# Kernel optimization log

Measured on AMD Instinct MI355X. Metric: run time of the kernel, lower is better.

## Reference

```python
import jax, jax.numpy as jnp
import numpy as np

D_MODEL = 1024
N_HEADS = 16
HEAD_DIM = D_MODEL // N_HEADS
D_FF = 4 * D_MODEL
LN_EPS = 1e-5  # torch nn.LayerNorm default


def setup_inputs() -> dict:
    key = jax.random.key(0)
    ks = jax.random.split(key, 6)
    B, T = 2, 2048
    s = lambda fan_in: 1.0 / np.sqrt(fan_in)
    return {
        "x": jax.random.normal(ks[0], (B, T, D_MODEL), dtype=jnp.float32),
        # weights stored as [in, out]
        "w_qkv": jax.random.normal(ks[1], (D_MODEL, 3 * D_MODEL), dtype=jnp.float32) * s(D_MODEL),
        "w_proj": jax.random.normal(ks[2], (D_MODEL, D_MODEL), dtype=jnp.float32) * s(D_MODEL),
        "ln1_g": jnp.ones((D_MODEL,), jnp.float32),
        "ln1_b": jnp.zeros((D_MODEL,), jnp.float32),
        "ln2_g": jnp.ones((D_MODEL,), jnp.float32),
        "ln2_b": jnp.zeros((D_MODEL,), jnp.float32),
        "w_ff1": jax.random.normal(ks[3], (D_MODEL, D_FF), dtype=jnp.float32) * s(D_MODEL),
        "b_ff1": jnp.zeros((D_FF,), jnp.float32),
        "w_ff2": jax.random.normal(ks[4], (D_FF, D_MODEL), dtype=jnp.float32) * s(D_FF),
        "b_ff2": jnp.zeros((D_MODEL,), jnp.float32),
    }


def _layernorm(x, g, b):
    mu = jnp.mean(x, axis=-1, keepdims=True)
    var = jnp.mean(jnp.square(x - mu), axis=-1, keepdims=True)
    return (x - mu) * jax.lax.rsqrt(var + LN_EPS) * g + b


def _attention(x, w_qkv, w_proj):
    B, T, C = x.shape
    qkv = x @ w_qkv  # [B,T,3C]
    q, k, v = jnp.split(qkv, 3, axis=-1)
    # [B, H, T, Dh]
    q = q.reshape(B, T, N_HEADS, HEAD_DIM).transpose(0, 2, 1, 3)
    k = k.reshape(B, T, N_HEADS, HEAD_DIM).transpose(0, 2, 1, 3)
    v = v.reshape(B, T, N_HEADS, HEAD_DIM).transpose(0, 2, 1, 3)
    att = jnp.einsum("bhqd,bhkd->bhqk", q, k) / np.sqrt(HEAD_DIM).astype(np.float32)
    causal = jnp.tril(jnp.ones((T, T), dtype=bool))
    att = jnp.where(causal, att, -jnp.inf)
    att = jax.nn.softmax(att, axis=-1)
    y = jnp.einsum("bhqk,bhkd->bhqd", att, v)
    y = y.transpose(0, 2, 1, 3).reshape(B, T, C)
    return y @ w_proj


def _ffn(x, w1, b1, w2, b2):
    h = jax.nn.gelu(x @ w1 + b1, approximate=False)  # torch nn.GELU default is exact
    return h @ w2 + b2


def reference(x, w_qkv, w_proj, ln1_g, ln1_b, ln2_g, ln2_b, w_ff1, b_ff1, w_ff2, b_ff2):
    x = x + _attention(_layernorm(x, ln1_g, ln1_b), w_qkv, w_proj)
    x = x + _ffn(_layernorm(x, ln2_g, ln2_b), w_ff1, b_ff1, w_ff2, b_ff2)
    return x
```

## Files before the change

### kernel.cpp

```cpp
#include <hip/hip_runtime.h>
#include <hip/hip_bf16.h>

typedef unsigned short u16;
typedef unsigned int u32;
typedef unsigned long long u64;
typedef __bf16 bf16x8 __attribute__((ext_vector_type(8)));
typedef float f32x4 __attribute__((ext_vector_type(4)));
typedef u16 u16x8 __attribute__((ext_vector_type(8)));

#define LN_EPS 1e-5f
#define SCALE_L2E 0.18033688011112042f

__device__ inline float bf2f(u16 u) { return __uint_as_float(((u32)u) << 16); }
__device__ inline u16 f2b(float f) {
    u32 u = __float_as_uint(f);
    u32 r = (u + 0x7fffu + ((u >> 16) & 1u)) >> 16;
    return (u16)r;
}
__device__ inline u32 cvtpk(float a, float b) {
    u32 r;
    asm("v_cvt_pk_bf16_f32 %0, %1, %2" : "=v"(r) : "v"(a), "v"(b));
    return r;
}

typedef __attribute__((address_space(3))) u32 as3_u32;
typedef const __attribute__((address_space(1))) u32 as1_u32;
__device__ inline void gl_lds16(const u16* g, u16* l) {
    __builtin_amdgcn_global_load_lds((as1_u32*)g, (as3_u32*)l, 16, 0, 0);
}

__global__ __launch_bounds__(256) void cast_transpose_k(const float* __restrict__ W,
                                                        u16* __restrict__ WT, int K, int N) {
    __shared__ float tile[64][65];
    int n0 = blockIdx.x * 64, k0 = blockIdx.y * 64;
    int t = threadIdx.x;
#pragma unroll
    for (int i = 0; i < 4; i++) {
        int idx = t + i * 256;
        int r = idx >> 4;
        int cq = idx & 15;
        float4 v = *reinterpret_cast<const float4*>(&W[(size_t)(k0 + r) * N + n0 + cq * 4]);
        tile[r][cq * 4 + 0] = v.x; tile[r][cq * 4 + 1] = v.y;
        tile[r][cq * 4 + 2] = v.z; tile[r][cq * 4 + 3] = v.w;
    }
    __syncthreads();
#pragma unroll
    for (int i = 0; i < 2; i++) {
        int c = t + i * 256;
        int n = c >> 3;
        int k8 = (c & 7) * 8;
        u16x8 o;
#pragma unroll
        for (int j = 0; j < 8; j++) o[j] = f2b(tile[k8 + j][n]);
        *reinterpret_cast<u16x8*>(&WT[(size_t)(n0 + n) * K + k0 + k8]) = o;
    }
}

__global__ __launch_bounds__(256) void layernorm_k(const float* __restrict__ X,
                                                   const float* __restrict__ g,
                                                   const float* __restrict__ b,
                                                   u16* __restrict__ out) {
    int row = blockIdx.x;
    int t = threadIdx.x;
    float4 v = *reinterpret_cast<const float4*>(&X[(size_t)row * 1024 + t * 4]);
    float s = v.x + v.y + v.z + v.w;
    float s2 = v.x * v.x + v.y * v.y + v.z * v.z + v.w * v.w;
#pragma unroll
    for (int o = 1; o < 64; o <<= 1) {
        s += __shfl_xor(s, o, 64);
        s2 += __shfl_xor(s2, o, 64);
    }
    __shared__ float ws[4], ws2[4];
    int wid = t >> 6, lane = t & 63;
    if (lane == 0) { ws[wid] = s; ws2[wid] = s2; }
    __syncthreads();
    float ts = ws[0] + ws[1] + ws[2] + ws[3];
    float ts2 = ws2[0] + ws2[1] + ws2[2] + ws2[3];
    float mu = ts * (1.0f / 1024.0f);
    float var = ts2 * (1.0f / 1024.0f) - mu * mu;
    float rs = rsqrtf(var + LN_EPS);
    float4 gg = *reinterpret_cast<const float4*>(&g[t * 4]);
    float4 bb = *reinterpret_cast<const float4*>(&b[t * 4]);
    u16 o4[4];
    o4[0] = f2b((v.x - mu) * rs * gg.x + bb.x);
    o4[1] = f2b((v.y - mu) * rs * gg.y + bb.y);
    o4[2] = f2b((v.z - mu) * rs * gg.z + bb.z);
    o4[3] = f2b((v.w - mu) * rs * gg.w + bb.w);
    *reinterpret_cast<ulonglong1*>(&out[(size_t)row * 1024 + t * 4]) =
        *reinterpret_cast<ulonglong1*>(o4);
}

template<int BN>
__global__ __launch_bounds__(256) void gemm_k(const u16* __restrict__ A,
                                              const u16* __restrict__ Bt,
                                              int M, int N, int K,
                                              const float* __restrict__ bias,
                                              const float* __restrict__ resid,
                                              int do_gelu,
                                              float* __restrict__ outF,
                                              u16* __restrict__ outB) {
    constexpr int NI = BN / 32;
    __shared__ u16 As[2][128 * 32];
    __shared__ u16 Bs[2][BN * 32];
    int gx = gridDim.x;
    int nwg = gx * gridDim.y;
    int id = blockIdx.y * gx + blockIdx.x;
    int id2 = (nwg & 7) ? id : ((id & 7) * (nwg >> 3) + (id >> 3));
    int bx = id2 % gx, by = id2 / gx;
    int m0 = by * 128, n0 = bx * BN;
    int t = threadIdx.x;
    int w = t >> 6, lane = t & 63;
    int lr = lane & 15, lg = lane >> 4;
    int wm = (w >> 1) * 64, wn = (w & 1) * (BN / 2);
    f32x4 acc[4][NI] = {};

    auto stage = [&](int buf, int k0) {
#pragma unroll
        for (int i = 0; i < 2; i++) {
            int c = t + i * 256;
            int row = c >> 2, pch = c & 3;
            gl_lds16(&A[(size_t)(m0 + row) * K + k0 + ((pch ^ ((row >> 1) & 3)) * 8)],
                     &As[buf][c * 8]);
        }
#pragma unroll
        for (int i = 0; i < BN / 64; i++) {
            int c = t + i * 256;
            int row = c >> 2, pch = c & 3;
            gl_lds16(&Bt[(size_t)(n0 + row) * K + k0 + ((pch ^ ((row >> 1) & 3)) * 8)],
                     &Bs[buf][c * 8]);
        }
    };

    stage(0, 0);
    __syncthreads();
    int cur = 0;
    for (int k0 = 0; k0 < K; k0 += 32) {
        if (k0 + 32 < K) stage(cur ^ 1, k0 + 32);
        bf16x8 af[4], bfr[NI];
#pragma unroll
        for (int mi = 0; mi < 4; mi++) {
            int row = wm + mi * 16 + lr;
            af[mi] = *reinterpret_cast<const bf16x8*>(&As[cur][row * 32 + ((lg ^ ((row >> 1) & 3)) * 8)]);
        }
#pragma unroll
        for (int ni = 0; ni < NI; ni++) {
            int row = wn + ni * 16 + lr;
            bfr[ni] = *reinterpret_cast<const bf16x8*>(&Bs[cur][row * 32 + ((lg ^ ((row >> 1) & 3)) * 8)]);
        }
        __builtin_amdgcn_s_setprio(1);
#pragma unroll
        for (int mi = 0; mi < 4; mi++)
#pragma unroll
            for (int ni = 0; ni < NI; ni++)
                acc[mi][ni] = __builtin_amdgcn_mfma_f32_16x16x32_bf16(af[mi], bfr[ni], acc[mi][ni], 0, 0, 0);
        __builtin_amdgcn_s_setprio(0);
        __syncthreads();
        cur ^= 1;
    }
#pragma unroll
    for (int mi = 0; mi < 4; mi++) {
#pragma unroll
        for (int ni = 0; ni < NI; ni++) {
            int col = n0 + wn + ni * 16 + lr;
#pragma unroll
            for (int i = 0; i < 4; i++) {
                int row = m0 + wm + mi * 16 + lg * 4 + i;
                float v = acc[mi][ni][i];
                if (bias) v += bias[col];
                if (do_gelu) v = 0.5f * v * (1.0f + erff(v * 0.70710678118f));
                if (resid) v += resid[(size_t)row * N + col];
                if (outF) outF[(size_t)row * N + col] = v;
                else outB[(size_t)row * N + col] = f2b(v);
            }
        }
    }
}

__global__ __launch_bounds__(256) void attn_k(const u16* __restrict__ QKV, u16* __restrict__ Y) {
    __shared__ u16 Ks[64 * 64];
    __shared__ u16 Vt[64 * 64];
    __shared__ u16 Pt[4][16 * 64];
    int u = (blockIdx.x + blockIdx.y) & 31;
    int vv = (u & 8) ? (u ^ 7) : u;
    int qt = 31 - vv;
    int bh = blockIdx.y;
    int b = bh >> 4, h = bh & 15;
    int t = threadIdx.x;
    int w = t >> 6, lane = t & 63;
    int lr = lane & 15, lg = lane >> 4;
    int q_g = qt * 64 + w * 16 + lr;
    size_t bhbase = (size_t)b * 2048 * 3072 + h * 64;

    bf16x8 qf[2];
#pragma unroll
    for (int ks = 0; ks < 2; ks++)
        qf[ks] = *reinterpret_cast<const bf16x8*>(&QKV[bhbase + (size_t)q_g * 3072 + ks * 32 + lg * 8]);

    float m = -1e30f, l = 0.0f;
    f32x4 oacc[4] = {};

    int vkey = t & 63;
    int vd0 = (t >> 6) * 8;
    int nkv = qt + 1;

    for (int kt = 0; kt < nkv; kt++) {
        size_t tb = bhbase + (size_t)(kt * 64) * 3072;
#pragma unroll
        for (int i = 0; i < 2; i++) {
            int c = t + i * 256;
            int key = c >> 3, pch = c & 7;
            gl_lds16(&QKV[tb + (size_t)key * 3072 + 1024 + ((pch ^ (key & 7)) * 8)], &Ks[c * 8]);
        }
        u16x8 vreg[2];
#pragma unroll
        for (int i = 0; i < 2; i++)
            vreg[i] = *reinterpret_cast<const u16x8*>(&QKV[tb + (size_t)vkey * 3072 + 2048 + vd0 + i * 32]);
#pragma unroll
        for (int i = 0; i < 2; i++)
#pragma unroll
            for (int j = 0; j < 8; j++) {
                int d = vd0 + i * 32 + j;
                Vt[(d * 64 + vkey) ^ ((d & 7) << 3)] = vreg[i][j];
            }
        __syncthreads();

        int kbmax = (kt == qt) ? (w + 1) : 4;
        f32x4 s[4];
        __builtin_amdgcn_s_setprio(1);
#pragma unroll
        for (int kb = 0; kb < 4; kb++) {
            if (kb < kbmax) {
                int key = kb * 16 + lr;
                bf16x8 k0 = *reinterpret_cast<const bf16x8*>(&Ks[key * 64 + ((lg ^ (key & 7)) * 8)]);
                bf16x8 k1 = *reinterpret_cast<const bf16x8*>(&Ks[key * 64 + (((4 + lg) ^ (key & 7)) * 8)]);
                f32x4 z = {0, 0, 0, 0};
                z = __builtin_amdgcn_mfma_f32_16x16x32_bf16(k0, qf[0], z, 0, 0, 0);
                s[kb] = __builtin_amdgcn_mfma_f32_16x16x32_bf16(k1, qf[1], z, 0, 0, 0);
            }
        }
        __builtin_amdgcn_s_setprio(0);

        float p[16];
        float mt = -1e30f;
        bool diag = (kt == qt);
#pragma unroll
        for (int kb = 0; kb < 4; kb++) {
            if (kb < kbmax) {
#pragma unroll
                for (int i2 = 0; i2 < 4; i2++) {
                    float v = s[kb][i2] * SCALE_L2E;
                    if (diag && kb == w)
                        v = (kb * 16 + lg * 4 + i2 <= w * 16 + lr) ? v : -1e30f;
                    p[kb * 4 + i2] = v;
                    mt = fmaxf(mt, v);
                }
            }
        }
        mt = fmaxf(mt, __shfl_xor(mt, 16, 64));
        mt = fmaxf(mt, __shfl_xor(mt, 32, 64));
        float mn = fmaxf(m, mt);
        float scf = exp2f(m - mn);
        float ps = 0.0f;
#pragma unroll
        for (int kb = 0; kb < 4; kb++) {
            if (kb < kbmax) {
#pragma unroll
                for (int i2 = 0; i2 < 4; i2++) {
                    float e = exp2f(p[kb * 4 + i2] - mn);
                    p[kb * 4 + i2] = e;
                    ps += e;
                }
            }
        }
        ps += __shfl_xor(ps, 16, 64);
        ps += __shfl_xor(ps, 32, 64);
        l = l * scf + ps;
        m = mn;
#pragma unroll
        for (int db = 0; db < 4; db++) {
            oacc[db][0] *= scf; oacc[db][1] *= scf;
            oacc[db][2] *= scf; oacc[db][3] *= scf;
        }
#pragma unroll
        for (int kb = 0; kb < 4; kb++) {
            u32 d0 = 0, d1 = 0;
            if (kb < kbmax) {
                d0 = cvtpk(p[kb * 4 + 0], p[kb * 4 + 1]);
                d1 = cvtpk(p[kb * 4 + 2], p[kb * 4 + 3]);
            }
            int eidx = (lr * 64 + kb * 16 + lg * 4) ^ ((lr & 7) << 3);
            *reinterpret_cast<u64*>(&Pt[w][eidx]) = (u64)d0 | ((u64)d1 << 32);
        }
        __builtin_amdgcn_s_setprio(1);
#pragma unroll
        for (int ks = 0; ks < 2; ks++) {
            bf16x8 pb = *reinterpret_cast<const bf16x8*>(&Pt[w][(lr * 64 + ks * 32 + lg * 8) ^ ((lr & 7) << 3)]);
#pragma unroll
            for (int db = 0; db < 4; db++) {
                int d = db * 16 + lr;
                bf16x8 va = *reinterpret_cast<const bf16x8*>(&Vt[(d * 64 + ks * 32 + lg * 8) ^ ((d & 7) << 3)]);
                oacc[db] = __builtin_amdgcn_mfma_f32_16x16x32_bf16(va, pb, oacc[db], 0, 0, 0);
            }
        }
        __builtin_amdgcn_s_setprio(0);
        __syncthreads();
    }

    float inv = 1.0f / l;
#pragma unroll
    for (int db = 0; db < 4; db++) {
        u32 lo = cvtpk(oacc[db][0] * inv, oacc[db][1] * inv);
        u32 hi = cvtpk(oacc[db][2] * inv, oacc[db][3] * inv);
        size_t ya = (size_t)(b * 2048 + q_g) * 1024 + h * 64 + db * 16 + lg * 4;
        *reinterpret_cast<u32*>(&Y[ya]) = lo;
        *reinterpret_cast<u32*>(&Y[ya + 2]) = hi;
    }
}

extern "C" void kernel_launch(void* const* d_in, const int* in_sizes, int n_in,
                              void* d_out, int out_size, void* d_ws, size_t ws_size,
                              hipStream_t stream) {
    const float* x      = (const float*)d_in[0];
    const float* w_qkv  = (const float*)d_in[1];
    const float* w_proj = (const float*)d_in[2];
    const float* ln1_g  = (const float*)d_in[3];
    const float* ln1_b  = (const float*)d_in[4];
    const float* ln2_g  = (const float*)d_in[5];
    const float* ln2_b  = (const float*)d_in[6];
    const float* w_ff1  = (const float*)d_in[7];
    const float* b_ff1  = (const float*)d_in[8];
    const float* w_ff2  = (const float*)d_in[9];
    const float* b_ff2  = (const float*)d_in[10];
    float* out = (float*)d_out;

    char* ws = (char*)d_ws;
    u16* qkv    = (u16*)(ws);
    u16* act16  = (u16*)(ws + 25165824);
    float* x2   = (float*)(ws + 33554432);
    u16* hbuf   = (u16*)(ws + 50331648);
    u16* wqkvT  = (u16*)(ws + 83886080);
    u16* wprojT = (u16*)(ws + 90177536);
    u16* wff1T  = (u16*)(ws + 92274688);
    u16* wff2T  = (u16*)(ws + 100663296);

    cast_transpose_k<<<dim3(48, 16), 256, 0, stream>>>(w_qkv, wqkvT, 1024, 3072);
    cast_transpose_k<<<dim3(16, 16), 256, 0, stream>>>(w_proj, wprojT, 1024, 1024);
    cast_transpose_k<<<dim3(64, 16), 256, 0, stream>>>(w_ff1, wff1T, 1024, 4096);
    cast_transpose_k<<<dim3(16, 64), 256, 0, stream>>>(w_ff2, wff2T, 4096, 1024);

    layernorm_k<<<4096, 256, 0, stream>>>(x, ln1_g, ln1_b, act16);
    gemm_k<128><<<dim3(24, 32), 256, 0, stream>>>(act16, wqkvT, 4096, 3072, 1024,
                                                  nullptr, nullptr, 0, nullptr, qkv);
    attn_k<<<dim3(32, 32), 256, 0, stream>>>(qkv, act16);
    gemm_k<64><<<dim3(16, 32), 256, 0, stream>>>(act16, wprojT, 4096, 1024, 1024,
                                                 nullptr, x, 0, x2, nullptr);
    layernorm_k<<<4096, 256, 0, stream>>>(x2, ln2_g, ln2_b, act16);
    gemm_k<128><<<dim3(32, 32), 256, 0, stream>>>(act16, wff1T, 4096, 4096, 1024,
                                                  b_ff1, nullptr, 1, nullptr, hbuf);
    gemm_k<64><<<dim3(16, 32), 256, 0, stream>>>(hbuf, wff2T, 4096, 1024, 4096,
                                                 b_ff2, x2, 0, out, nullptr);
}
```

Baseline: 353.7 us.

## Double-buffer K/V tiles in attention and skip rescale when max barely changes

The attention kernel now double-buffers its K and V shared-memory tiles. The next tile's global loads are issued before the current tile's compute, and the V transpose-scatter is deferred to the end of the iteration, which cuts one barrier per tile and hides load latency. It also adds a lazy softmax rescale: the running max and accumulator rescale are updated only when some lane's new max exceeds the old one by more than 8 in the log2 domain. This doubles K/V shared-memory use, which may lower occupancy, and allows exponentials up to 2^8 before rescaling, which stays safe in fp32.

```diff
diff --git a/kernel.cpp b/kernel.cpp
--- a/kernel.cpp
+++ b/kernel.cpp
@@ -177,8 +177,8 @@
 }
 
 __global__ __launch_bounds__(256) void attn_k(const u16* __restrict__ QKV, u16* __restrict__ Y) {
-    __shared__ u16 Ks[64 * 64];
-    __shared__ u16 Vt[64 * 64];
+    __shared__ u16 Ks[2][64 * 64];
+    __shared__ u16 Vt[2][64 * 64];
     __shared__ u16 Pt[4][16 * 64];
     int u = (blockIdx.x + blockIdx.y) & 31;
     int vv = (u & 8) ? (u ^ 7) : u;
@@ -203,26 +203,48 @@
     int vd0 = (t >> 6) * 8;
     int nkv = qt + 1;
 
-    for (int kt = 0; kt < nkv; kt++) {
-        size_t tb = bhbase + (size_t)(kt * 64) * 3072;
+    auto stageK = [&](int buf, int kt2) {
+        size_t tb = bhbase + (size_t)(kt2 * 64) * 3072;
 #pragma unroll
         for (int i = 0; i < 2; i++) {
             int c = t + i * 256;
             int key = c >> 3, pch = c & 7;
-            gl_lds16(&QKV[tb + (size_t)key * 3072 + 1024 + ((pch ^ (key & 7)) * 8)], &Ks[c * 8]);
-        }
-        u16x8 vreg[2];
+            gl_lds16(&QKV[tb + (size_t)key * 3072 + 1024 + ((pch ^ (key & 7)) * 8)],
+                     &Ks[buf][c * 8]);
+        }
+    };
+    auto loadV = [&](u16x8* vr, int kt2) {
+        size_t tb = bhbase + (size_t)(kt2 * 64) * 3072;
 #pragma unroll
         for (int i = 0; i < 2; i++)
-            vreg[i] = *reinterpret_cast<const u16x8*>(&QKV[tb + (size_t)vkey * 3072 + 2048 + vd0 + i * 32]);
+            vr[i] = *reinterpret_cast<const u16x8*>(&QKV[tb + (size_t)vkey * 3072 + 2048 + vd0 + i * 32]);
+    };
+    auto scatterV = [&](int buf, u16x8* vr) {
 #pragma unroll
         for (int i = 0; i < 2; i++)
 #pragma unroll
             for (int j = 0; j < 8; j++) {
                 int d = vd0 + i * 32 + j;
-                Vt[(d * 64 + vkey) ^ ((d & 7) << 3)] = vreg[i][j];
-            }
-        __syncthreads();
+                Vt[buf][(d * 64 + vkey) ^ ((d & 7) << 3)] = vr[i][j];
+            }
+    };
+
+    {
+        u16x8 v0[2];
+        loadV(v0, 0);
+        stageK(0, 0);
+        scatterV(0, v0);
+    }
+    __syncthreads();
+    int cur = 0;
+
+    for (int kt = 0; kt < nkv; kt++) {
+        bool hn = (kt + 1 < nkv);
+        u16x8 vnx[2];
+        if (hn) {
+            loadV(vnx, kt + 1);
+            stageK(cur ^ 1, kt + 1);
+        }
 
         int kbmax = (kt == qt) ? (w + 1) : 4;
         f32x4 s[4];
@@ -231,8 +253,8 @@
         for (int kb = 0; kb < 4; kb++) {
             if (kb < kbmax) {
                 int key = kb * 16 + lr;
-                bf16x8 k0 = *reinterpret_cast<const bf16x8*>(&Ks[key * 64 + ((lg ^ (key & 7)) * 8)]);
-                bf16x8 k1 = *reinterpret_cast<const bf16x8*>(&Ks[key * 64 + (((4 + lg) ^ (key & 7)) * 8)]);
+                bf16x8 k0 = *reinterpret_cast<const bf16x8*>(&Ks[cur][key * 64 + ((lg ^ (key & 7)) * 8)]);
+                bf16x8 k1 = *reinterpret_cast<const bf16x8*>(&Ks[cur][key * 64 + (((4 + lg) ^ (key & 7)) * 8)]);
                 f32x4 z = {0, 0, 0, 0};
                 z = __builtin_amdgcn_mfma_f32_16x16x32_bf16(k0, qf[0], z, 0, 0, 0);
                 s[kb] = __builtin_amdgcn_mfma_f32_16x16x32_bf16(k1, qf[1], z, 0, 0, 0);
@@ -258,15 +280,24 @@
         }
         mt = fmaxf(mt, __shfl_xor(mt, 16, 64));
         mt = fmaxf(mt, __shfl_xor(mt, 32, 64));
-        float mn = fmaxf(m, mt);
-        float scf = exp2f(m - mn);
+        if (!__all(mt <= m + 8.0f)) {
+            float mn = fmaxf(m, mt);
+            float scf = exp2f(m - mn);
+            l *= scf;
+#pragma unroll
+            for (int db = 0; db < 4; db++) {
+                oacc[db][0] *= scf; oacc[db][1] *= scf;
+                oacc[db][2] *= scf; oacc[db][3] *= scf;
+            }
+            m = mn;
+        }
         float ps = 0.0f;
 #pragma unroll
         for (int kb = 0; kb < 4; kb++) {
             if (kb < kbmax) {
 #pragma unroll
                 for (int i2 = 0; i2 < 4; i2++) {
-                    float e = exp2f(p[kb * 4 + i2] - mn);
+                    float e = exp2f(p[kb * 4 + i2] - m);
                     p[kb * 4 + i2] = e;
                     ps += e;
                 }
@@ -274,13 +305,7 @@
         }
         ps += __shfl_xor(ps, 16, 64);
         ps += __shfl_xor(ps, 32, 64);
-        l = l * scf + ps;
-        m = mn;
-#pragma unroll
-        for (int db = 0; db < 4; db++) {
-            oacc[db][0] *= scf; oacc[db][1] *= scf;
-            oacc[db][2] *= scf; oacc[db][3] *= scf;
-        }
+        l += ps;
 #pragma unroll
         for (int kb = 0; kb < 4; kb++) {
             u32 d0 = 0, d1 = 0;
@@ -298,12 +323,15 @@
 #pragma unroll
             for (int db = 0; db < 4; db++) {
                 int d = db * 16 + lr;
-                bf16x8 va = *reinterpret_cast<const bf16x8*>(&Vt[(d * 64 + ks * 32 + lg * 8) ^ ((d & 7) << 3)]);
+                bf16x8 va = *reinterpret_cast<const bf16x8*>(&Vt[cur][(d * 64 + ks * 32 + lg * 8) ^ ((d & 7) << 3)]);
                 oacc[db] = __builtin_amdgcn_mfma_f32_16x16x32_bf16(va, pb, oacc[db], 0, 0, 0);
             }
         }
         __builtin_amdgcn_s_setprio(0);
+
+        if (hn) scatterV(cur ^ 1, vnx);
         __syncthreads();
+        cur ^= 1;
     }
 
     float inv = 1.0f / l;
```

New measurement: 357.0 us. Within noise of the previous version (+0.9%).

## Add 256x256 tile GEMM kernel for QKV and FF1 projections

Applied to the files above, without the earlier changes.

Introduces a 512-thread GEMM with 256x256 output tiles, K-step 64, XOR-swizzled LDS staging and double buffering, used for the QKV and FF1 matmuls. Larger tiles raise arithmetic intensity and reduce global/L2 traffic per FLOP. In exchange the block count drops below the CU count for QKV, LDS usage limits occupancy to one block per CU, and the epilogue uses scalar bf16 stores.

```diff
diff --git a/kernel.cpp b/kernel.cpp
--- a/kernel.cpp
+++ b/kernel.cpp
@@ -88,6 +88,94 @@
     o4[3] = f2b((v.w - mu) * rs * gg.w + bb.w);
     *reinterpret_cast<ulonglong1*>(&out[(size_t)row * 1024 + t * 4]) =
         *reinterpret_cast<ulonglong1*>(o4);
+}
+
+__global__ __launch_bounds__(512, 2) void gemm256_k(const u16* __restrict__ A,
+                                                    const u16* __restrict__ Bt,
+                                                    int M, int N, int K,
+                                                    const float* __restrict__ bias,
+                                                    int do_gelu,
+                                                    u16* __restrict__ outB) {
+    __shared__ u16 As[2][256 * 64];
+    __shared__ u16 Bs[2][256 * 64];
+    int gx = gridDim.x;
+    int nwg = gx * gridDim.y;
+    int id = blockIdx.y * gx + blockIdx.x;
+    int id2 = (nwg & 7) ? id : ((id & 7) * (nwg >> 3) + (id >> 3));
+    int bx = id2 % gx, by = id2 / gx;
+    int m0 = by * 256, n0 = bx * 256;
+    int t = threadIdx.x;
+    int w = t >> 6, lane = t & 63;
+    int lr = lane & 15, lg = lane >> 4;
+    int wm = (w >> 2) * 128, wn = (w & 3) * 64;
+    f32x4 acc[8][4] = {};
+
+    auto stage = [&](int buf, int kt) {
+        int k0 = kt * 64;
+#pragma unroll
+        for (int i = 0; i < 4; i++) {
+            int c = t + i * 512;
+            int row = c >> 3, pch = c & 7;
+            gl_lds16(&A[(size_t)(m0 + row) * K + k0 + ((pch ^ (row & 7)) * 8)],
+                     &As[buf][c * 8]);
+        }
+#pragma unroll
+        for (int i = 0; i < 4; i++) {
+            int c = t + i * 512;
+            int row = c >> 3, pch = c & 7;
+            gl_lds16(&Bt[(size_t)(n0 + row) * K + k0 + ((pch ^ (row & 7)) * 8)],
+                     &Bs[buf][c * 8]);
+        }
+    };
+
+    int nk = K >> 6;
+    stage(0, 0);
+    __syncthreads();
+    for (int kt = 0; kt < nk; kt++) {
+        int cur = kt & 1;
+        if (kt + 1 < nk) stage(cur ^ 1, kt + 1);
+#pragma unroll
+        for (int ks = 0; ks < 2; ks++) {
+            bf16x8 af[8], bfr[4];
+#pragma unroll
+            for (int mi = 0; mi < 8; mi++) {
+                int row = wm + mi * 16 + lr;
+                af[mi] = *reinterpret_cast<const bf16x8*>(
+                    &As[cur][row * 64 + (((ks * 4 + lg) ^ (row & 7)) * 8)]);
+            }
+#pragma unroll
+            for (int ni = 0; ni < 4; ni++) {
+                int row = wn + ni * 16 + lr;
+                bfr[ni] = *reinterpret_cast<const bf16x8*>(
+                    &Bs[cur][row * 64 + (((ks * 4 + lg) ^ (row & 7)) * 8)]);
+            }
+            __builtin_amdgcn_s_setprio(1);
+#pragma unroll
+            for (int mi = 0; mi < 8; mi++)
+#pragma unroll
+                for (int ni = 0; ni < 4; ni++)
+                    acc[mi][ni] = __builtin_amdgcn_mfma_f32_16x16x32_bf16(
+                        af[mi], bfr[ni], acc[mi][ni], 0, 0, 0);
+            __builtin_amdgcn_s_setprio(0);
+        }
+        __syncthreads();
+    }
+
+#pragma unroll
+    for (int mi = 0; mi < 8; mi++) {
+#pragma unroll
+        for (int ni = 0; ni < 4; ni++) {
+            int col = n0 + wn + ni * 16 + lr;
+#pragma unroll
+            for (int i = 0; i < 4; i++) {
+                int row = m0 + wm + mi * 16 + lg * 4 + i;
+                float v = acc[mi][ni][i];
+                if (bias) v += bias[col];
+                if (do_gelu) v = 0.5f * v * (1.0f + erff(v * 0.70710678118f));
+                outB[(size_t)row * N + col] = f2b(v);
+            }
+        }
+    }
 }
 
 template<int BN>
@@ -349,14 +437,14 @@
     cast_transpose_k<<<dim3(16, 64), 256, 0, stream>>>(w_ff2, wff2T, 4096, 1024);
 
     layernorm_k<<<4096, 256, 0, stream>>>(x, ln1_g, ln1_b, act16);
-    gemm_k<128><<<dim3(24, 32), 256, 0, stream>>>(act16, wqkvT, 4096, 3072, 1024,
-                                                  nullptr, nullptr, 0, nullptr, qkv);
+    gemm256_k<<<dim3(12, 16), 512, 0, stream>>>(act16, wqkvT, 4096, 3072, 1024,
+                                                nullptr, 0, qkv);
     attn_k<<<dim3(32, 32), 256, 0, stream>>>(qkv, act16);
     gemm_k<64><<<dim3(16, 32), 256, 0, stream>>>(act16, wprojT, 4096, 1024, 1024,
                                                  nullptr, x, 0, x2, nullptr);
     layernorm_k<<<4096, 256, 0, stream>>>(x2, ln2_g, ln2_b, act16);
-    gemm_k<128><<<dim3(32, 32), 256, 0, stream>>>(act16, wff1T, 4096, 4096, 1024,
-                                                  b_ff1, nullptr, 1, nullptr, hbuf);
+    gemm256_k<<<dim3(16, 16), 512, 0, stream>>>(act16, wff1T, 4096, 4096, 1024,
+                                                b_ff1, 1, hbuf);
     gemm_k<64><<<dim3(16, 32), 256, 0, stream>>>(hbuf, wff2T, 4096, 1024, 4096,
                                                  b_ff2, x2, 0, out, nullptr);
 }
```

After: 347.5 us. Within noise of the previous version (-1.8%).
